# Kernel tuning notes

Measured on AMD Instinct MI355X. Metric: run time of the kernel, lower is better.

Reference implementation:

```python
import jax, jax.numpy as jnp
import numpy as np

KERNEL_BANDWIDTH = 0.3
STEP_SIZE = 0.5
NB_ITERATIONS = 4


def setup_inputs() -> dict:
    key = jax.random.key(0)
    # B x D x H x W pixel embeddings
    x_in = jax.random.normal(key, (2, 64, 96, 96), dtype=jnp.float32)
    return {"x_in": x_in}


def reference(x_in):
    B, D, H, W = x_in.shape
    N = H * W
    x0 = x_in.reshape(B, D, N)

    def body(x, _):
        # Gaussian-like kernel K[i,j] = exp(bw * <x_i, x_j>), symmetric NxN per batch
        K = jnp.exp(KERNEL_BANDWIDTH * jnp.einsum('bdn,bdm->bnm', x, x))  # (B,N,N)
        # torch: diag(K^T @ 1) then inverse of that diagonal == 1/column-sums
        colsum = jnp.sum(K, axis=1)  # (B,N)
        # x @ (K diag(1/colsum)): column-normalized weighted mean of embeddings
        xk = jnp.einsum('bdn,bnm->bdm', x, K) / colsum[:, None, :]
        x_new = STEP_SIZE * xk + (1.0 - STEP_SIZE) * x
        return x_new, x_new

    _, ys = jax.lax.scan(body, x0, None, length=NB_ITERATIONS)  # (I,B,D,N)
    allx = jnp.concatenate([x0[None], ys], axis=0)  # (I+1,B,D,N)
    # B x (I+1) x D x H x W
    return jnp.transpose(allx, (1, 0, 2, 3)).reshape(B, NB_ITERATIONS + 1, D, H, W)
```

## Files before the change

kernel.cpp:

```cpp
#include <hip/hip_runtime.h>
#include <hip/hip_bf16.h>

constexpr int B_    = 2;
constexpr int N_    = 9216;
constexpr int ITERS = 4;

constexpr int MTQ     = 128;
constexpr int MBF     = N_ / MTQ;
constexpr int KS      = 4;
constexpr int KEYS_WG = N_ / KS;
constexpr int KT      = 64;
constexpr int KTILES  = KEYS_WG / KT;
constexpr int NWG     = B_ * MBF * KS;
constexpr int PB      = 144;
constexpr int CGRID   = B_ * (N_ / 32);

constexpr float STEP = 0.5f;
constexpr float C2   = 0.43280851226668905f;

using short8   = __attribute__((ext_vector_type(8))) short;
using float16v = __attribute__((ext_vector_type(16))) float;
typedef __attribute__((ext_vector_type(2))) __bf16 bf16x2;

__device__ __forceinline__ unsigned short f2bf(float f) {
  union { float f; unsigned u; } v; v.f = f;
  unsigned u = v.u;
  unsigned r = (u + 0x7fffu + ((u >> 16) & 1u)) >> 16;
  return (unsigned short)r;
}

#if __has_builtin(__builtin_amdgcn_cvt_pk_bf16_f32)
__device__ __forceinline__ unsigned pk2bf(float a, float b) {
  bf16x2 r = __builtin_amdgcn_cvt_pk_bf16_f32(a, b);
  union { bf16x2 h; unsigned u; } v; v.h = r; return v.u;
}
#else
__device__ __forceinline__ unsigned pk2bf(float a, float b) {
  return (unsigned)f2bf(a) | ((unsigned)f2bf(b) << 16);
}
#endif

__device__ __forceinline__ float csum2(unsigned u, float cs) {
#if __has_builtin(__builtin_amdgcn_fdot2_f32_bf16)
  union { unsigned x; bf16x2 h; } a, o;
  a.x = u; o.x = 0x3f803f80u;
  return __builtin_amdgcn_fdot2_f32_bf16(a.h, o.h, cs, false);
#else
  union { unsigned u; float f; } lo, hi;
  lo.u = u << 16; hi.u = u & 0xffff0000u;
  return cs + lo.f + hi.f;
#endif
}

__device__ __forceinline__ void dma16(const unsigned short* g,
                                      unsigned short* lds_base, int lane) {
#if __has_builtin(__builtin_amdgcn_global_load_lds)
  __builtin_amdgcn_global_load_lds(
      (const __attribute__((address_space(1))) unsigned int*)g,
      (__attribute__((address_space(3))) unsigned int*)lds_base, 16, 0, 0);
#else
  *(int4*)((char*)lds_base + lane * 16) = *(const int4*)g;
#endif
}

__global__ void prep_kernel(const float* __restrict__ xin, float* __restrict__ out,
                            unsigned short* __restrict__ XT,
                            unsigned short* __restrict__ Xbf)
{
  const int bx = blockIdx.x;
  const int nb = bx % PB, b = bx / PB;
  const int n0 = nb * 64;
  const int tid = threadIdx.x;
  __shared__ float tile[64 * 65];

  #pragma unroll
  for (int r = 0; r < 16; ++r) {
    int idx = r * 256 + tid;
    int d = idx >> 6, j = idx & 63;
    float v = xin[((size_t)b * 64 + d) * N_ + n0 + j];
    out[(((size_t)b * 5 + 0) * 64 + d) * N_ + n0 + j] = v;
    Xbf[((size_t)b * 64 + d) * N_ + n0 + j] = f2bf(v);
    tile[d * 65 + j] = v;
  }
  __syncthreads();
  #pragma unroll
  for (int r = 0; r < 16; ++r) {
    int idx = r * 256 + tid;
    int nl = idx >> 6, d = idx & 63;
    XT[((size_t)b * N_ + n0 + nl) * 64 + d] = f2bf(tile[d * 65 + nl]);
  }
}

__global__ void __launch_bounds__(256, 3) flash_kernel(
    const unsigned short* __restrict__ XT,
    const unsigned short* __restrict__ Xbf,
    float* __restrict__ pacc, float* __restrict__ pcs)
{
  const int bx   = blockIdx.x;
  const int ks   = bx & 3;
  const int mb   = (bx >> 2) % MBF;
  const int b    = bx / (MBF * KS);
  const int tid  = threadIdx.x;
  const int wave = tid >> 6, lane = tid & 63;
  const int c = lane & 31, h = lane >> 5;
  const int cp = (c & 0x13) | ((c & 4) << 1) | ((c & 8) >> 1);
  const int m0 = mb * MTQ;
  const int bpaddr = (lane ^ 32) << 2;

  const unsigned short* XTb = XT  + (size_t)b * N_ * 64;
  const unsigned short* Xb  = Xbf + (size_t)b * 64 * N_;

  __shared__ __align__(16) unsigned short sXT[2][KT * 64];
  __shared__ __align__(16) unsigned short sXB[2][64 * KT];

  const int rr = lane >> 3, sc = lane & 7;
  const int gc = sc ^ rr;

  const int n0g0 = ks * KEYS_WG;

  const unsigned short* xtp  = XTb + (size_t)(n0g0 + wave * 16 + rr) * 64 + gc * 8;
  const unsigned short* xbp0 = Xb  + (size_t)(wave * 16 + rr) * N_ + n0g0 + gc * 8;
  const unsigned short* xbp1 = xbp0 + (size_t)8 * N_;

  auto stage = [&](int buf, const unsigned short* xt_,
                   const unsigned short* xb0_, const unsigned short* xb1_) {
    unsigned short* lt = &sXT[buf][wave * 16 * 64];
    unsigned short* lb = &sXB[buf][wave * 16 * 64];
    dma16(xt_,       lt,       lane);
    dma16(xt_ + 512, lt + 512, lane);
    dma16(xb0_,      lb,       lane);
    dma16(xb1_,      lb + 512, lane);
  };

  stage(0, xtp, xbp0, xbp1);
  xtp += KT * 64; xbp0 += KT; xbp1 += KT;

  short8 qf[4];
  #pragma unroll
  for (int k = 0; k < 4; ++k) {
    short8 raw = *(const short8*)(XTb +
        (size_t)(m0 + wave * 32 + c) * 64 + k * 16 + h * 8);
    unsigned o[4];
    const unsigned* rw = (const unsigned*)&raw;
    #pragma unroll
    for (int p4 = 0; p4 < 4; ++p4) {
      union { unsigned u; float f; } lo, hi;
      lo.u = rw[p4] << 16; hi.u = rw[p4] & 0xffff0000u;
      o[p4] = pk2bf(lo.f * C2, hi.f * C2);
    }
    qf[k] = *(const short8*)o;
  }

  const int e = cp & 7;
  const unsigned short* afb[4];
  #pragma unroll
  for (int k = 0; k < 4; ++k)
    afb[k] = &sXT[0][cp * 64 + ((2 * k + h) ^ e) * 8];
  const int ec = c & 7;
  const unsigned short* bfb0[2], * bfb1[2];
  #pragma unroll
  for (int s = 0; s < 2; ++s) {
    bfb0[s] = &sXB[0][c * 64 + ((4 * s +     h) ^ ec) * 8];
    bfb1[s] = &sXB[0][c * 64 + ((4 * s + 2 + h) ^ ec) * 8];
  }

  float16v zv;
  #pragma unroll
  for (int p = 0; p < 16; ++p) zv[p] = 0.f;
  float16v acc[2];
  acc[0] = zv; acc[1] = zv;
  float cs = 0.f;

  __syncthreads();

  #pragma unroll 2
  for (int t = 0; t < KTILES; ++t) {
    const int buf = t & 1;
    if (t + 1 < KTILES) {
      stage(buf ^ 1, xtp, xbp0, xbp1);
      xtp += KT * 64; xbp0 += KT; xbp1 += KT;
    }

    #pragma unroll
    for (int s = 0; s < 2; ++s) {
      short8 af[4];
      #pragma unroll
      for (int k = 0; k < 4; ++k)
        af[k] = *(const short8*)(afb[k] + buf * 4096 + s * 2048);

      float16v S = zv;
      #pragma unroll
      for (int k = 0; k < 4; ++k)
        S = __builtin_amdgcn_mfma_f32_32x32x16_bf16(af[k], qf[k], S, 0, 0, 0);

      unsigned q[8];
      #pragma unroll
      for (int g = 0; g < 8; ++g) {
        float w0 = __builtin_amdgcn_exp2f(S[2 * g]);
        float w1 = __builtin_amdgcn_exp2f(S[2 * g + 1]);
        unsigned u = pk2bf(w0, w1);
        q[g] = u;
        cs = csum2(u, cs);
      }

      union { unsigned d[4]; short8 s8; } a20, a21;
      a20.d[0] = q[0]; a20.d[1] = q[1]; a20.d[2] = q[2]; a20.d[3] = q[3];
      a21.d[0] = q[4]; a21.d[1] = q[5]; a21.d[2] = q[6]; a21.d[3] = q[7];

      short8 b20[2], b21[2];
      #pragma unroll
      for (int dt = 0; dt < 2; ++dt) {
        b20[dt] = *(const short8*)(bfb0[s] + buf * 4096 + dt * 2048);
        b21[dt] = *(const short8*)(bfb1[s] + buf * 4096 + dt * 2048);
      }
      #pragma unroll
      for (int dt = 0; dt < 2; ++dt)
        acc[dt] = __builtin_amdgcn_mfma_f32_32x32x16_bf16(a20.s8, b20[dt], acc[dt], 0, 0, 0);
      #pragma unroll
      for (int dt = 0; dt < 2; ++dt)
        acc[dt] = __builtin_amdgcn_mfma_f32_32x32x16_bf16(a21.s8, b21[dt], acc[dt], 0, 0, 0);
    }

    __syncthreads();
  }

  union { float f; int i; } cu; cu.f = cs;
  cu.i = __builtin_amdgcn_ds_bpermute(bpaddr, cu.i);
  float cst = cs + cu.f;
  if (h == 0) pcs[(size_t)bx * 128 + wave * 32 + c] = cst;

  float* pw = pacc + (size_t)bx * (MTQ * 64);
  #pragma unroll
  for (int dt = 0; dt < 2; ++dt)
    #pragma unroll
    for (int p = 0; p < 16; ++p) {
      int m = wave * 32 + (p & 3) + 8 * (p >> 2) + 4 * h;
      pw[m * 64 + dt * 32 + c] = acc[dt][p];
    }
}

__global__ void combine_kernel(const float* __restrict__ pacc,
                               const float* __restrict__ pcs,
                               float* __restrict__ out,
                               unsigned short* __restrict__ XT,
                               unsigned short* __restrict__ Xbf, int t)
{
  const int bx  = blockIdx.x;
  const int q32 = bx % 288, b = bx / 288;
  const int m0  = q32 * 32;
  const int base = (b * MBF + (q32 >> 2)) * KS;
  const int poff = (q32 & 3) * 2048;
  const int coff = (q32 & 3) * 32;
  const int tid = threadIdx.x;
  __shared__ float accs[32 * 65];
  __shared__ float cstl[32];

  #pragma unroll
  for (int r = 0; r < 2; ++r) {
    int i4 = r * 256 + tid;
    float4 s = make_float4(0.f, 0.f, 0.f, 0.f);
    #pragma unroll
    for (int k = 0; k < KS; ++k) {
      const float4* p = (const float4*)(pacc + (size_t)(base + k) * 8192 + poff);
      float4 v = p[i4];
      s.x += v.x; s.y += v.y; s.z += v.z; s.w += v.w;
    }
    int m = i4 >> 4, d0 = (i4 & 15) * 4;
    accs[m * 65 + d0 + 0] = s.x;
    accs[m * 65 + d0 + 1] = s.y;
    accs[m * 65 + d0 + 2] = s.z;
    accs[m * 65 + d0 + 3] = s.w;
  }
  if (tid < 32) {
    float cv = 0.f;
    #pragma unroll
    for (int k = 0; k < KS; ++k) cv += pcs[(size_t)(base + k) * 128 + coff + tid];
    cstl[tid] = cv;
  }
  __syncthreads();

  #pragma unroll
  for (int r = 0; r < 4; ++r) {
    int idx = r * 256 + tid;
    int ml = (idx & 15) * 2, d = idx >> 4;
    float a0 = accs[ml * 65 + d], a1 = accs[(ml + 1) * 65 + d];
    size_t obase = (((size_t)b * 5 + t) * 64 + d) * N_ + m0 + ml;
    float2 xc = *(const float2*)(out + obase);
    float v0 = STEP * (a0 / cstl[ml])     + (1.f - STEP) * xc.x;
    float v1 = STEP * (a1 / cstl[ml + 1]) + (1.f - STEP) * xc.y;
    *(float2*)(out + obase + (size_t)64 * N_) = make_float2(v0, v1);
    *(unsigned*)(Xbf + ((size_t)b * 64 + d) * N_ + m0 + ml) = pk2bf(v0, v1);
    accs[ml * 65 + d] = v0; accs[(ml + 1) * 65 + d] = v1;
  }
  __syncthreads();

  #pragma unroll
  for (int r = 0; r < 4; ++r) {
    int idx = r * 256 + tid;
    int m = idx >> 5, d = (idx & 31) * 2;
    *(unsigned*)(XT + ((size_t)b * N_ + m0 + m) * 64 + d)
        = pk2bf(accs[m * 65 + d], accs[m * 65 + d + 1]);
  }
}

extern "C" void kernel_launch(void* const* d_in, const int* in_sizes, int n_in,
                              void* d_out, int out_size, void* d_ws, size_t ws_size,
                              hipStream_t stream)
{
  (void)in_sizes; (void)n_in; (void)out_size; (void)ws_size;
  const float* xin = (const float*)d_in[0];
  float* out = (float*)d_out;
  char* ws = (char*)d_ws;

  unsigned short* XT  = (unsigned short*)(ws);
  unsigned short* Xbf = (unsigned short*)(ws +  2359296);
  float*          pacc = (float*)(ws +  4718592);
  float*          pcs  = (float*)(ws + 23592960);

  prep_kernel<<<B_ * PB, 256, 0, stream>>>(xin, out, XT, Xbf);
  for (int t = 0; t < ITERS; ++t) {
    flash_kernel<<<NWG, 256, 0, stream>>>(XT, Xbf, pacc, pcs);
    combine_kernel<<<CGRID, 256, 0, stream>>>(pacc, pcs, out, XT, Xbf, t);
  }
}
```

Before: 373.8 us.

## Split key tile across two wave groups with 512-thread blocks and LDS reduction

Doubles the flash kernel block to 8 waves. Each pair of waves shares a 32-query slice and splits the 64-key tile into two 32-key halves, so each wave does half the per-tile work. The two halves' accumulators and column sums are reduced through shared memory at the end. Each wave now issues one DMA per tile instead of two, and the column-sum accumulation is split into two chains to shorten dependencies. This aims for more latency hiding and parallelism per CU, at the cost of a final LDS reduction, an extra barrier, and higher register pressure under launch_bounds(512,6).

```diff
diff --git a/kernel.cpp b/kernel.cpp
--- a/kernel.cpp
+++ b/kernel.cpp
@@ -91,7 +91,7 @@
   }
 }
 
-__global__ void __launch_bounds__(256, 3) flash_kernel(
+__global__ void __launch_bounds__(512, 6) flash_kernel(
     const unsigned short* __restrict__ XT,
     const unsigned short* __restrict__ Xbf,
     float* __restrict__ pacc, float* __restrict__ pcs)
@@ -102,6 +102,7 @@
   const int b    = bx / (MBF * KS);
   const int tid  = threadIdx.x;
   const int wave = tid >> 6, lane = tid & 63;
+  const int qw   = wave & 3, kh = wave >> 2;
   const int c = lane & 31, h = lane >> 5;
   const int cp = (c & 0x13) | ((c & 4) << 1) | ((c & 8) >> 1);
   const int m0 = mb * MTQ;
@@ -112,34 +113,29 @@
 
   __shared__ __align__(16) unsigned short sXT[2][KT * 64];
   __shared__ __align__(16) unsigned short sXB[2][64 * KT];
+  __shared__ float csred[256];
 
   const int rr = lane >> 3, sc = lane & 7;
   const int gc = sc ^ rr;
 
   const int n0g0 = ks * KEYS_WG;
 
-  const unsigned short* xtp  = XTb + (size_t)(n0g0 + wave * 16 + rr) * 64 + gc * 8;
-  const unsigned short* xbp0 = Xb  + (size_t)(wave * 16 + rr) * N_ + n0g0 + gc * 8;
-  const unsigned short* xbp1 = xbp0 + (size_t)8 * N_;
-
-  auto stage = [&](int buf, const unsigned short* xt_,
-                   const unsigned short* xb0_, const unsigned short* xb1_) {
-    unsigned short* lt = &sXT[buf][wave * 16 * 64];
-    unsigned short* lb = &sXB[buf][wave * 16 * 64];
-    dma16(xt_,       lt,       lane);
-    dma16(xt_ + 512, lt + 512, lane);
-    dma16(xb0_,      lb,       lane);
-    dma16(xb1_,      lb + 512, lane);
+  const unsigned short* xtp = XTb + (size_t)(n0g0 + wave * 8 + rr) * 64 + gc * 8;
+  const unsigned short* xbp = Xb  + (size_t)(wave * 8 + rr) * N_ + n0g0 + gc * 8;
+
+  auto stage = [&](int buf, const unsigned short* xt_, const unsigned short* xb_) {
+    dma16(xt_, &sXT[buf][wave * 512], lane);
+    dma16(xb_, &sXB[buf][wave * 512], lane);
   };
 
-  stage(0, xtp, xbp0, xbp1);
-  xtp += KT * 64; xbp0 += KT; xbp1 += KT;
+  stage(0, xtp, xbp);
+  xtp += KT * 64; xbp += KT;
 
   short8 qf[4];
   #pragma unroll
   for (int k = 0; k < 4; ++k) {
     short8 raw = *(const short8*)(XTb +
-        (size_t)(m0 + wave * 32 + c) * 64 + k * 16 + h * 8);
+        (size_t)(m0 + qw * 32 + c) * 64 + k * 16 + h * 8);
     unsigned o[4];
     const unsigned* rw = (const unsigned*)&raw;
     #pragma unroll
@@ -155,21 +151,17 @@
   const unsigned short* afb[4];
   #pragma unroll
   for (int k = 0; k < 4; ++k)
-    afb[k] = &sXT[0][cp * 64 + ((2 * k + h) ^ e) * 8];
+    afb[k] = &sXT[0][(kh * 32 + cp) * 64 + ((2 * k + h) ^ e) * 8];
   const int ec = c & 7;
-  const unsigned short* bfb0[2], * bfb1[2];
-  #pragma unroll
-  for (int s = 0; s < 2; ++s) {
-    bfb0[s] = &sXB[0][c * 64 + ((4 * s +     h) ^ ec) * 8];
-    bfb1[s] = &sXB[0][c * 64 + ((4 * s + 2 + h) ^ ec) * 8];
-  }
+  const unsigned short* bfb0 = &sXB[0][c * 64 + ((4 * kh +     h) ^ ec) * 8];
+  const unsigned short* bfb1 = &sXB[0][c * 64 + ((4 * kh + 2 + h) ^ ec) * 8];
 
   float16v zv;
   #pragma unroll
   for (int p = 0; p < 16; ++p) zv[p] = 0.f;
   float16v acc[2];
   acc[0] = zv; acc[1] = zv;
-  float cs = 0.f;
+  float cs0 = 0.f, cs1 = 0.f;
 
   __syncthreads();
 
@@ -177,66 +169,93 @@
   for (int t = 0; t < KTILES; ++t) {
     const int buf = t & 1;
     if (t + 1 < KTILES) {
-      stage(buf ^ 1, xtp, xbp0, xbp1);
-      xtp += KT * 64; xbp0 += KT; xbp1 += KT;
-    }
-
-    #pragma unroll
-    for (int s = 0; s < 2; ++s) {
-      short8 af[4];
+      stage(buf ^ 1, xtp, xbp);
+      xtp += KT * 64; xbp += KT;
+    }
+
+    short8 af[4];
+    #pragma unroll
+    for (int k = 0; k < 4; ++k)
+      af[k] = *(const short8*)(afb[k] + buf * 4096);
+
+    float16v S = zv;
+    #pragma unroll
+    for (int k = 0; k < 4; ++k)
+      S = __builtin_amdgcn_mfma_f32_32x32x16_bf16(af[k], qf[k], S, 0, 0, 0);
+
+    unsigned q[8];
+    #pragma unroll
+    for (int g = 0; g < 8; ++g) {
+      float w0 = __builtin_amdgcn_exp2f(S[2 * g]);
+      float w1 = __builtin_amdgcn_exp2f(S[2 * g + 1]);
+      unsigned u = pk2bf(w0, w1);
+      q[g] = u;
+      if (g & 1) cs1 = csum2(u, cs1); else cs0 = csum2(u, cs0);
+    }
+
+    union { unsigned d[4]; short8 s8; } a20, a21;
+    a20.d[0] = q[0]; a20.d[1] = q[1]; a20.d[2] = q[2]; a20.d[3] = q[3];
+    a21.d[0] = q[4]; a21.d[1] = q[5]; a21.d[2] = q[6]; a21.d[3] = q[7];
+
+    short8 b20[2], b21[2];
+    #pragma unroll
+    for (int dt = 0; dt < 2; ++dt) {
+      b20[dt] = *(const short8*)(bfb0 + buf * 4096 + dt * 2048);
+      b21[dt] = *(const short8*)(bfb1 + buf * 4096 + dt * 2048);
+    }
+    #pragma unroll
+    for (int dt = 0; dt < 2; ++dt)
+      acc[dt] = __builtin_amdgcn_mfma_f32_32x32x16_bf16(a20.s8, b20[dt], acc[dt], 0, 0, 0);
+    #pragma unroll
+    for (int dt = 0; dt < 2; ++dt)
+      acc[dt] = __builtin_amdgcn_mfma_f32_32x32x16_bf16(a21.s8, b21[dt], acc[dt], 0, 0, 0);
+
+    __syncthreads();
+  }
+
+  float cs = cs0 + cs1;
+
+  float4* red4 = (qw < 2) ? ((float4*)&sXT[0][0]) + qw * 512
+                          : ((float4*)&sXB[0][0]) + (qw - 2) * 512;
+
+  if (kh == 1) {
+    #pragma unroll
+    for (int dt = 0; dt < 2; ++dt)
       #pragma unroll
-      for (int k = 0; k < 4; ++k)
-        af[k] = *(const short8*)(afb[k] + buf * 4096 + s * 2048);
-
-      float16v S = zv;
+      for (int j = 0; j < 4; ++j) {
+        float4 v;
+        v.x = acc[dt][4 * j + 0]; v.y = acc[dt][4 * j + 1];
+        v.z = acc[dt][4 * j + 2]; v.w = acc[dt][4 * j + 3];
+        red4[(dt * 4 + j) * 64 + lane] = v;
+      }
+    csred[qw * 64 + lane] = cs;
+  }
+  __syncthreads();
+  if (kh == 0) {
+    #pragma unroll
+    for (int dt = 0; dt < 2; ++dt)
       #pragma unroll
-      for (int k = 0; k < 4; ++k)
-        S = __builtin_amdgcn_mfma_f32_32x32x16_bf16(af[k], qf[k], S, 0, 0, 0);
-
-      unsigned q[8];
+      for (int j = 0; j < 4; ++j) {
+        float4 v = red4[(dt * 4 + j) * 64 + lane];
+        acc[dt][4 * j + 0] += v.x; acc[dt][4 * j + 1] += v.y;
+        acc[dt][4 * j + 2] += v.z; acc[dt][4 * j + 3] += v.w;
+      }
+    cs += csred[qw * 64 + lane];
+
+    union { float f; int i; } cu; cu.f = cs;
+    cu.i = __builtin_amdgcn_ds_bpermute(bpaddr, cu.i);
+    float cst = cs + cu.f;
+    if (h == 0) pcs[(size_t)bx * 128 + qw * 32 + c] = cst;
+
+    float* pw = pacc + (size_t)bx * (MTQ * 64);
+    #pragma unroll
+    for (int dt = 0; dt < 2; ++dt)
       #pragma unroll
-      for (int g = 0; g < 8; ++g) {
-        float w0 = __builtin_amdgcn_exp2f(S[2 * g]);
-        float w1 = __builtin_amdgcn_exp2f(S[2 * g + 1]);
-        unsigned u = pk2bf(w0, w1);
-        q[g] = u;
-        cs = csum2(u, cs);
+      for (int p = 0; p < 16; ++p) {
+        int m = qw * 32 + (p & 3) + 8 * (p >> 2) + 4 * h;
+        pw[m * 64 + dt * 32 + c] = acc[dt][p];
       }
-
-      union { unsigned d[4]; short8 s8; } a20, a21;
-      a20.d[0] = q[0]; a20.d[1] = q[1]; a20.d[2] = q[2]; a20.d[3] = q[3];
-      a21.d[0] = q[4]; a21.d[1] = q[5]; a21.d[2] = q[6]; a21.d[3] = q[7];
-
-      short8 b20[2], b21[2];
-      #pragma unroll
-      for (int dt = 0; dt < 2; ++dt) {
-        b20[dt] = *(const short8*)(bfb0[s] + buf * 4096 + dt * 2048);
-        b21[dt] = *(const short8*)(bfb1[s] + buf * 4096 + dt * 2048);
-      }
-      #pragma unroll
-      for (int dt = 0; dt < 2; ++dt)
-        acc[dt] = __builtin_amdgcn_mfma_f32_32x32x16_bf16(a20.s8, b20[dt], acc[dt], 0, 0, 0);
-      #pragma unroll
-      for (int dt = 0; dt < 2; ++dt)
-        acc[dt] = __builtin_amdgcn_mfma_f32_32x32x16_bf16(a21.s8, b21[dt], acc[dt], 0, 0, 0);
-    }
-
-    __syncthreads();
-  }
-
-  union { float f; int i; } cu; cu.f = cs;
-  cu.i = __builtin_amdgcn_ds_bpermute(bpaddr, cu.i);
-  float cst = cs + cu.f;
-  if (h == 0) pcs[(size_t)bx * 128 + wave * 32 + c] = cst;
-
-  float* pw = pacc + (size_t)bx * (MTQ * 64);
-  #pragma unroll
-  for (int dt = 0; dt < 2; ++dt)
-    #pragma unroll
-    for (int p = 0; p < 16; ++p) {
-      int m = wave * 32 + (p & 3) + 8 * (p >> 2) + 4 * h;
-      pw[m * 64 + dt * 32 + c] = acc[dt][p];
-    }
+  }
 }
 
 __global__ void combine_kernel(const float* __restrict__ pacc,
@@ -319,7 +338,7 @@
 
   prep_kernel<<<B_ * PB, 256, 0, stream>>>(xin, out, XT, Xbf);
   for (int t = 0; t < ITERS; ++t) {
-    flash_kernel<<<NWG, 256, 0, stream>>>(XT, Xbf, pacc, pcs);
+    flash_kernel<<<NWG, 512, 0, stream>>>(XT, Xbf, pacc, pcs);
     combine_kernel<<<CGRID, 256, 0, stream>>>(pacc, pcs, out, XT, Xbf, t);
   }
 }
```

Result: slower. 692.3 us (+85.2%).

## Software-pipeline exp weights into next tile's PV MFMAs with triple-buffered LDS

Applied to the files above, without the earlier changes.

Restructures the key-tile loop so the P·V MFMAs for tile t-1 run at the start of iteration t, overlapping them with the QK MFMAs and exp2 work of tile t. The exp-weight packs are carried across iterations in registers, and LDS moves to triple buffering so the previous tile's X data stays valid while the next one is staged. Raised wave priority around the deferred MFMAs and split column-sum accumulators are added. The cost is more register pressure and LDS use, which may reduce occupancy.

```diff
diff --git a/kernel.cpp b/kernel.cpp
--- a/kernel.cpp
+++ b/kernel.cpp
@@ -110,8 +110,8 @@
   const unsigned short* XTb = XT  + (size_t)b * N_ * 64;
   const unsigned short* Xb  = Xbf + (size_t)b * 64 * N_;
 
-  __shared__ __align__(16) unsigned short sXT[2][KT * 64];
-  __shared__ __align__(16) unsigned short sXB[2][64 * KT];
+  __shared__ __align__(16) unsigned short sXT[3][KT * 64];
+  __shared__ __align__(16) unsigned short sXB[3][64 * KT];
 
   const int rr = lane >> 3, sc = lane & 7;
   const int gc = sc ^ rr;
@@ -169,16 +169,46 @@
   for (int p = 0; p < 16; ++p) zv[p] = 0.f;
   float16v acc[2];
   acc[0] = zv; acc[1] = zv;
-  float cs = 0.f;
+  float cs0 = 0.f, cs1 = 0.f;
+
+  unsigned qwp[2][8];
+  #pragma unroll
+  for (int s = 0; s < 2; ++s)
+    #pragma unroll
+    for (int g = 0; g < 8; ++g) qwp[s][g] = 0;
 
   __syncthreads();
 
-  #pragma unroll 2
+  #pragma unroll 3
   for (int t = 0; t < KTILES; ++t) {
-    const int buf = t & 1;
+    const int buf = t % 3;
     if (t + 1 < KTILES) {
-      stage(buf ^ 1, xtp, xbp0, xbp1);
+      stage((t + 1) % 3, xtp, xbp0, xbp1);
       xtp += KT * 64; xbp0 += KT; xbp1 += KT;
+    }
+
+    if (t > 0) {
+      const int pb = (t + 2) % 3;
+      __builtin_amdgcn_s_setprio(1);
+      #pragma unroll
+      for (int s = 0; s < 2; ++s) {
+        union { unsigned d[4]; short8 s8; } a20, a21;
+        #pragma unroll
+        for (int j = 0; j < 4; ++j) { a20.d[j] = qwp[s][j]; a21.d[j] = qwp[s][4 + j]; }
+        short8 b20[2], b21[2];
+        #pragma unroll
+        for (int dt = 0; dt < 2; ++dt) {
+          b20[dt] = *(const short8*)(bfb0[s] + pb * 4096 + dt * 2048);
+          b21[dt] = *(const short8*)(bfb1[s] + pb * 4096 + dt * 2048);
+        }
+        #pragma unroll
+        for (int dt = 0; dt < 2; ++dt)
+          acc[dt] = __builtin_amdgcn_mfma_f32_32x32x16_bf16(a20.s8, b20[dt], acc[dt], 0, 0, 0);
+        #pragma unroll
+        for (int dt = 0; dt < 2; ++dt)
+          acc[dt] = __builtin_amdgcn_mfma_f32_32x32x16_bf16(a21.s8, b21[dt], acc[dt], 0, 0, 0);
+      }
+      __builtin_amdgcn_s_setprio(0);
     }
 
     #pragma unroll
@@ -193,25 +223,31 @@
       for (int k = 0; k < 4; ++k)
         S = __builtin_amdgcn_mfma_f32_32x32x16_bf16(af[k], qf[k], S, 0, 0, 0);
 
-      unsigned q[8];
       #pragma unroll
       for (int g = 0; g < 8; ++g) {
         float w0 = __builtin_amdgcn_exp2f(S[2 * g]);
         float w1 = __builtin_amdgcn_exp2f(S[2 * g + 1]);
         unsigned u = pk2bf(w0, w1);
-        q[g] = u;
-        cs = csum2(u, cs);
+        qwp[s][g] = u;
+        if (s) cs1 = csum2(u, cs1); else cs0 = csum2(u, cs0);
       }
-
+    }
+
+    __syncthreads();
+  }
+
+  {
+    constexpr int pb = (KTILES - 1) % 3;
+    #pragma unroll
+    for (int s = 0; s < 2; ++s) {
       union { unsigned d[4]; short8 s8; } a20, a21;
-      a20.d[0] = q[0]; a20.d[1] = q[1]; a20.d[2] = q[2]; a20.d[3] = q[3];
-      a21.d[0] = q[4]; a21.d[1] = q[5]; a21.d[2] = q[6]; a21.d[3] = q[7];
-
+      #pragma unroll
+      for (int j = 0; j < 4; ++j) { a20.d[j] = qwp[s][j]; a21.d[j] = qwp[s][4 + j]; }
       short8 b20[2], b21[2];
       #pragma unroll
       for (int dt = 0; dt < 2; ++dt) {
-        b20[dt] = *(const short8*)(bfb0[s] + buf * 4096 + dt * 2048);
-        b21[dt] = *(const short8*)(bfb1[s] + buf * 4096 + dt * 2048);
+        b20[dt] = *(const short8*)(bfb0[s] + pb * 4096 + dt * 2048);
+        b21[dt] = *(const short8*)(bfb1[s] + pb * 4096 + dt * 2048);
       }
       #pragma unroll
       for (int dt = 0; dt < 2; ++dt)
@@ -220,9 +256,8 @@
       for (int dt = 0; dt < 2; ++dt)
         acc[dt] = __builtin_amdgcn_mfma_f32_32x32x16_bf16(a21.s8, b21[dt], acc[dt], 0, 0, 0);
     }
-
-    __syncthreads();
-  }
+  }
+  float cs = cs0 + cs1;
 
   union { float f; int i; } cu; cu.f = cs;
   cu.i = __builtin_amdgcn_ds_bpermute(bpaddr, cu.i);
```

Result: no change. 375.4 us (+0.4%).

## Split flash kernel waves into 2x2 query/key grid with LDS reduction

Applied to the files above, without the earlier changes.

Each wave now handles two 32-row query tiles over half of each key tile instead of one query tile over the full key tile. Each A/B fragment loaded from LDS is reused across two query tiles, halving LDS fragment reads per MFMA. The cost is a cross-wave reduction of accumulators and column sums through shared memory at the end, and higher register use. Launch bounds drop occupancy from 3 to 2 blocks per CU to fit the doubled accumulators.

```diff
diff --git a/kernel.cpp b/kernel.cpp
--- a/kernel.cpp
+++ b/kernel.cpp
@@ -91,7 +91,7 @@
   }
 }
 
-__global__ void __launch_bounds__(256, 3) flash_kernel(
+__global__ void __launch_bounds__(256, 2) flash_kernel(
     const unsigned short* __restrict__ XT,
     const unsigned short* __restrict__ Xbf,
     float* __restrict__ pacc, float* __restrict__ pcs)
@@ -102,6 +102,7 @@
   const int b    = bx / (MBF * KS);
   const int tid  = threadIdx.x;
   const int wave = tid >> 6, lane = tid & 63;
+  const int qw   = wave & 1, kh = wave >> 1;
   const int c = lane & 31, h = lane >> 5;
   const int cp = (c & 0x13) | ((c & 4) << 1) | ((c & 8) >> 1);
   const int m0 = mb * MTQ;
@@ -135,41 +136,39 @@
   stage(0, xtp, xbp0, xbp1);
   xtp += KT * 64; xbp0 += KT; xbp1 += KT;
 
-  short8 qf[4];
-  #pragma unroll
-  for (int k = 0; k < 4; ++k) {
-    short8 raw = *(const short8*)(XTb +
-        (size_t)(m0 + wave * 32 + c) * 64 + k * 16 + h * 8);
-    unsigned o[4];
-    const unsigned* rw = (const unsigned*)&raw;
-    #pragma unroll
-    for (int p4 = 0; p4 < 4; ++p4) {
-      union { unsigned u; float f; } lo, hi;
-      lo.u = rw[p4] << 16; hi.u = rw[p4] & 0xffff0000u;
-      o[p4] = pk2bf(lo.f * C2, hi.f * C2);
-    }
-    qf[k] = *(const short8*)o;
-  }
+  short8 qf[2][4];
+  #pragma unroll
+  for (int qt = 0; qt < 2; ++qt)
+    #pragma unroll
+    for (int k = 0; k < 4; ++k) {
+      short8 raw = *(const short8*)(XTb +
+          (size_t)(m0 + qw * 64 + qt * 32 + c) * 64 + k * 16 + h * 8);
+      unsigned o[4];
+      const unsigned* rw = (const unsigned*)&raw;
+      #pragma unroll
+      for (int p4 = 0; p4 < 4; ++p4) {
+        union { unsigned u; float f; } lo, hi;
+        lo.u = rw[p4] << 16; hi.u = rw[p4] & 0xffff0000u;
+        o[p4] = pk2bf(lo.f * C2, hi.f * C2);
+      }
+      qf[qt][k] = *(const short8*)o;
+    }
 
   const int e = cp & 7;
   const unsigned short* afb[4];
   #pragma unroll
   for (int k = 0; k < 4; ++k)
-    afb[k] = &sXT[0][cp * 64 + ((2 * k + h) ^ e) * 8];
+    afb[k] = &sXT[0][(kh * 32 + cp) * 64 + ((2 * k + h) ^ e) * 8];
   const int ec = c & 7;
-  const unsigned short* bfb0[2], * bfb1[2];
-  #pragma unroll
-  for (int s = 0; s < 2; ++s) {
-    bfb0[s] = &sXB[0][c * 64 + ((4 * s +     h) ^ ec) * 8];
-    bfb1[s] = &sXB[0][c * 64 + ((4 * s + 2 + h) ^ ec) * 8];
-  }
+  const unsigned short* bfb0 = &sXB[0][c * 64 + ((4 * kh +     h) ^ ec) * 8];
+  const unsigned short* bfb1 = &sXB[0][c * 64 + ((4 * kh + 2 + h) ^ ec) * 8];
 
   float16v zv;
   #pragma unroll
   for (int p = 0; p < 16; ++p) zv[p] = 0.f;
-  float16v acc[2];
-  acc[0] = zv; acc[1] = zv;
-  float cs = 0.f;
+  float16v acc[2][2];
+  acc[0][0] = zv; acc[0][1] = zv; acc[1][0] = zv; acc[1][1] = zv;
+  float cs[2] = {0.f, 0.f};
 
   __syncthreads();
 
@@ -181,17 +180,24 @@
       xtp += KT * 64; xbp0 += KT; xbp1 += KT;
     }
 
-    #pragma unroll
-    for (int s = 0; s < 2; ++s) {
-      short8 af[4];
+    short8 af[4];
+    #pragma unroll
+    for (int k = 0; k < 4; ++k)
+      af[k] = *(const short8*)(afb[k] + buf * 4096);
+
+    short8 b20[2], b21[2];
+    #pragma unroll
+    for (int dt = 0; dt < 2; ++dt) {
+      b20[dt] = *(const short8*)(bfb0 + buf * 4096 + dt * 2048);
+      b21[dt] = *(const short8*)(bfb1 + buf * 4096 + dt * 2048);
+    }
+
+    #pragma unroll
+    for (int qt = 0; qt < 2; ++qt) {
+      float16v S = zv;
       #pragma unroll
       for (int k = 0; k < 4; ++k)
-        af[k] = *(const short8*)(afb[k] + buf * 4096 + s * 2048);
-
-      float16v S = zv;
-      #pragma unroll
-      for (int k = 0; k < 4; ++k)
-        S = __builtin_amdgcn_mfma_f32_32x32x16_bf16(af[k], qf[k], S, 0, 0, 0);
+        S = __builtin_amdgcn_mfma_f32_32x32x16_bf16(af[k], qf[qt][k], S, 0, 0, 0);
 
       unsigned q[8];
       #pragma unroll
@@ -200,43 +206,80 @@
         float w1 = __builtin_amdgcn_exp2f(S[2 * g + 1]);
         unsigned u = pk2bf(w0, w1);
         q[g] = u;
-        cs = csum2(u, cs);
+        cs[qt] = csum2(u, cs[qt]);
       }
 
       union { unsigned d[4]; short8 s8; } a20, a21;
       a20.d[0] = q[0]; a20.d[1] = q[1]; a20.d[2] = q[2]; a20.d[3] = q[3];
       a21.d[0] = q[4]; a21.d[1] = q[5]; a21.d[2] = q[6]; a21.d[3] = q[7];
 
-      short8 b20[2], b21[2];
-      #pragma unroll
-      for (int dt = 0; dt < 2; ++dt) {
-        b20[dt] = *(const short8*)(bfb0[s] + buf * 4096 + dt * 2048);
-        b21[dt] = *(const short8*)(bfb1[s] + buf * 4096 + dt * 2048);
-      }
+      acc[qt][0] = __builtin_amdgcn_mfma_f32_32x32x16_bf16(a20.s8, b20[0], acc[qt][0], 0, 0, 0);
+      acc[qt][1] = __builtin_amdgcn_mfma_f32_32x32x16_bf16(a20.s8, b20[1], acc[qt][1], 0, 0, 0);
+      acc[qt][0] = __builtin_amdgcn_mfma_f32_32x32x16_bf16(a21.s8, b21[0], acc[qt][0], 0, 0, 0);
+      acc[qt][1] = __builtin_amdgcn_mfma_f32_32x32x16_bf16(a21.s8, b21[1], acc[qt][1], 0, 0, 0);
+    }
+
+    __syncthreads();
+  }
+
+  float* csb = (float*)&sXT[0][0];
+  if (kh == 1) {
+    csb[qw * 128 + lane]      = cs[0];
+    csb[qw * 128 + 64 + lane] = cs[1];
+  }
+  __syncthreads();
+  if (kh == 0) {
+    cs[0] += csb[qw * 128 + lane];
+    cs[1] += csb[qw * 128 + 64 + lane];
+  }
+  __syncthreads();
+
+  float4* red4 = (qw == 0) ? (float4*)&sXT[0][0] : (float4*)&sXB[0][0];
+  if (kh == 1) {
+    #pragma unroll
+    for (int qt = 0; qt < 2; ++qt)
       #pragma unroll
       for (int dt = 0; dt < 2; ++dt)
-        acc[dt] = __builtin_amdgcn_mfma_f32_32x32x16_bf16(a20.s8, b20[dt], acc[dt], 0, 0, 0);
+        #pragma unroll
+        for (int j = 0; j < 4; ++j) {
+          float4 v;
+          v.x = acc[qt][dt][4 * j + 0]; v.y = acc[qt][dt][4 * j + 1];
+          v.z = acc[qt][dt][4 * j + 2]; v.w = acc[qt][dt][4 * j + 3];
+          red4[((qt * 2 + dt) * 4 + j) * 64 + lane] = v;
+        }
+  }
+  __syncthreads();
+  if (kh == 0) {
+    #pragma unroll
+    for (int qt = 0; qt < 2; ++qt)
       #pragma unroll
       for (int dt = 0; dt < 2; ++dt)
-        acc[dt] = __builtin_amdgcn_mfma_f32_32x32x16_bf16(a21.s8, b21[dt], acc[dt], 0, 0, 0);
-    }
-
-    __syncthreads();
-  }
-
-  union { float f; int i; } cu; cu.f = cs;
-  cu.i = __builtin_amdgcn_ds_bpermute(bpaddr, cu.i);
-  float cst = cs + cu.f;
-  if (h == 0) pcs[(size_t)bx * 128 + wave * 32 + c] = cst;
-
-  float* pw = pacc + (size_t)bx * (MTQ * 64);
-  #pragma unroll
-  for (int dt = 0; dt < 2; ++dt)
-    #pragma unroll
-    for (int p = 0; p < 16; ++p) {
-      int m = wave * 32 + (p & 3) + 8 * (p >> 2) + 4 * h;
-      pw[m * 64 + dt * 32 + c] = acc[dt][p];
-    }
+        #pragma unroll
+        for (int j = 0; j < 4; ++j) {
+          float4 v = red4[((qt * 2 + dt) * 4 + j) * 64 + lane];
+          acc[qt][dt][4 * j + 0] += v.x; acc[qt][dt][4 * j + 1] += v.y;
+          acc[qt][dt][4 * j + 2] += v.z; acc[qt][dt][4 * j + 3] += v.w;
+        }
+
+    #pragma unroll
+    for (int qt = 0; qt < 2; ++qt) {
+      union { float f; int i; } cu; cu.f = cs[qt];
+      cu.i = __builtin_amdgcn_ds_bpermute(bpaddr, cu.i);
+      float cst = cs[qt] + cu.f;
+      if (h == 0) pcs[(size_t)bx * 128 + qw * 64 + qt * 32 + c] = cst;
+    }
+
+    float* pw = pacc + (size_t)bx * (MTQ * 64);
+    #pragma unroll
+    for (int qt = 0; qt < 2; ++qt)
+      #pragma unroll
+      for (int dt = 0; dt < 2; ++dt)
+        #pragma unroll
+        for (int p = 0; p < 16; ++p) {
+          int m = qw * 64 + qt * 32 + (p & 3) + 8 * (p >> 2) + 4 * h;
+          pw[m * 64 + dt * 32 + c] = acc[qt][dt][p];
+        }
+  }
 }
 
 __global__ void combine_kernel(const float* __restrict__ pacc,
```

Result: slower. 415.9 us (+11.3%).
